# Kernel tuning notes

Hardware: AMD Instinct MI355X
Metric: run time of the kernel (lower is better)

Reference implementation:

```python
import jax, jax.numpy as jnp
import numpy as np

EDGE_THRESHOLD = 0.1
N_NODES, IN_DIM, OUT_DIM, EDGE_DIM = 512, 128, 128, 64
LN_EPS = 1e-5


def setup_inputs() -> dict:
    key = jax.random.key(0)
    ks = jax.random.split(key, 20)
    s = 0.05
    d_in2e = 2 * IN_DIM + EDGE_DIM
    return {
        "node_features": jax.random.normal(ks[0], (N_NODES, IN_DIM), jnp.float32),
        "W": jax.random.normal(ks[1], (N_NODES, N_NODES), jnp.float32),
        "M": jax.random.normal(ks[2], (N_NODES, N_NODES), jnp.float32),
        "edge_features": jax.random.normal(ks[3], (N_NODES, N_NODES, EDGE_DIM), jnp.float32),
        # node_mlp: Linear(in,out) -> ReLU -> Linear(out,out)
        "node_w1": jax.random.normal(ks[4], (IN_DIM, OUT_DIM), jnp.float32) * s,
        "node_b1": jnp.zeros((OUT_DIM,), jnp.float32),
        "node_w2": jax.random.normal(ks[5], (OUT_DIM, OUT_DIM), jnp.float32) * s,
        "node_b2": jnp.zeros((OUT_DIM,), jnp.float32),
        # directed_msg: Linear(2*in+edge_dim,out) -> ReLU -> Linear(out,out)
        "dir_w1": jax.random.normal(ks[6], (d_in2e, OUT_DIM), jnp.float32) * s,
        "dir_b1": jnp.zeros((OUT_DIM,), jnp.float32),
        "dir_w2": jax.random.normal(ks[7], (OUT_DIM, OUT_DIM), jnp.float32) * s,
        "dir_b2": jnp.zeros((OUT_DIM,), jnp.float32),
        # bidirected_msg: Linear(2*in,out) -> ReLU -> Linear(out,out)
        "bi_w1": jax.random.normal(ks[8], (2 * IN_DIM, OUT_DIM), jnp.float32) * s,
        "bi_b1": jnp.zeros((OUT_DIM,), jnp.float32),
        "bi_w2": jax.random.normal(ks[9], (OUT_DIM, OUT_DIM), jnp.float32) * s,
        "bi_b2": jnp.zeros((OUT_DIM,), jnp.float32),
        # LayerNorm(out)
        "ln_g": jnp.ones((OUT_DIM,), jnp.float32),
        "ln_b": jnp.zeros((OUT_DIM,), jnp.float32),
    }


def reference(node_features, W, M, edge_features,
              node_w1, node_b1, node_w2, node_b2,
              dir_w1, dir_b1, dir_w2, dir_b2,
              bi_w1, bi_b1, bi_w2, bi_b2,
              ln_g, ln_b):
    n, d = node_features.shape
    x = node_features

    # self path
    h_self = jax.nn.relu(x @ node_w1 + node_b1) @ node_w2 + node_b2

    # directed messages: msg[j,i] = MLP([x_j, x_i, e_{j,i}]), weight = |W[j,i]| masked.
    # First linear split by concat blocks to avoid materializing (n,n,2d+e).
    src = x @ dir_w1[:d]                 # (n,h)   parent/source term
    tgt = x @ dir_w1[d:2 * d]            # (n,h)   target term
    edg = jnp.einsum('jie,eh->jih', edge_features, dir_w1[2 * d:])  # (n,n,h)
    h1 = jax.nn.relu(src[:, None, :] + tgt[None, :, :] + edg + dir_b1)  # (n,n,h) [j,i]
    msg_d = h1 @ dir_w2 + dir_b2         # (n,n,out)
    absW = jnp.abs(W)
    wd = jnp.where(absW > EDGE_THRESHOLD, absW, 0.0)  # (n,n) [parent j, target i]
    h_dir = jnp.einsum('jio,ji->io', msg_d, wd)

    # bidirected messages: for node i, neighbors j: MLP([x_j, x_i]), weight = |M[i,j]| masked, j != i
    bsrc = x @ bi_w1[:d]
    btgt = x @ bi_w1[d:]
    h1b = jax.nn.relu(bsrc[:, None, :] + btgt[None, :, :] + bi_b1)  # (n,n,h) [j,i]
    msg_b = h1b @ bi_w2 + bi_b2
    absM = jnp.abs(M)
    wb = jnp.where(absM > EDGE_THRESHOLD, absM, 0.0)
    wb = wb * (1.0 - jnp.eye(n, dtype=wb.dtype))  # exclude self
    h_bi = jnp.einsum('jio,ij->io', msg_b, wb)

    h = h_self + h_dir + h_bi
    mu = jnp.mean(h, axis=-1, keepdims=True)
    var = jnp.mean(jnp.square(h - mu), axis=-1, keepdims=True)
    return (h - mu) * jax.lax.rsqrt(var + LN_EPS) * ln_g + ln_b
```

## Files before the change

### kernel.cpp

```cpp
#include <hip/hip_runtime.h>
#include <hip/hip_bf16.h>
#include <cstdint>

#define NN 512
#define DD 128
#define EE 64
#define THR 0.1f
#define NCHUNK 16

typedef __bf16 bf16x8 __attribute__((ext_vector_type(8)));
typedef float  f32x4  __attribute__((ext_vector_type(4)));

__global__ __launch_bounds__(256) void k_zero(float* __restrict__ p, int n)
{
    int i = blockIdx.x * 256 + threadIdx.x;
    if (i < n) p[i] = 0.f;
}

__global__ __launch_bounds__(128) void k_pre(
    const float* __restrict__ x,
    const float* __restrict__ dw1, const float* __restrict__ bw1,
    const float* __restrict__ nw1, const float* __restrict__ nb1,
    float* __restrict__ src, float* __restrict__ tgt,
    float* __restrict__ bsrc, float* __restrict__ btgt, float* __restrict__ hmid)
{
    const int i0 = blockIdx.x * 4;
    const int h  = threadIdx.x;
    const int which = blockIdx.y;
    const float* B; float* outp;
    switch (which) {
        case 0:  B = dw1;          outp = src;  break;
        case 1:  B = dw1 + DD*DD;  outp = tgt;  break;
        case 2:  B = bw1;          outp = bsrc; break;
        case 3:  B = bw1 + DD*DD;  outp = btgt; break;
        default: B = nw1;          outp = hmid; break;
    }
    __shared__ float sx[4][DD];
    for (int idx = h; idx < 4*DD; idx += DD)
        sx[idx >> 7][idx & 127] = x[i0*DD + idx];
    __syncthreads();
    float a0=0.f, a1=0.f, a2=0.f, a3=0.f;
    for (int k = 0; k < DD; ++k) {
        float w = B[k*DD + h];
        a0 = fmaf(sx[0][k], w, a0);
        a1 = fmaf(sx[1][k], w, a1);
        a2 = fmaf(sx[2][k], w, a2);
        a3 = fmaf(sx[3][k], w, a3);
    }
    if (which == 4) {
        float bb = nb1[h];
        a0 = fmaxf(a0+bb, 0.f); a1 = fmaxf(a1+bb, 0.f);
        a2 = fmaxf(a2+bb, 0.f); a3 = fmaxf(a3+bb, 0.f);
    }
    outp[(i0+0)*DD + h] = a0;
    outp[(i0+1)*DD + h] = a1;
    outp[(i0+2)*DD + h] = a2;
    outp[(i0+3)*DD + h] = a3;
}

__global__ __launch_bounds__(256, 2) void k_msg(
    const float* __restrict__ ef, const float* __restrict__ W,
    const float* __restrict__ M,
    const float* __restrict__ dw1, const float* __restrict__ db1,
    const float* __restrict__ src, const float* __restrict__ tgt,
    const float* __restrict__ bsrc, const float* __restrict__ btgt,
    const float* __restrict__ bb1,
    float* __restrict__ td_base, float* __restrict__ tb_base,
    float* __restrict__ wsum_d, float* __restrict__ wsum_b, int partial)
{
    __shared__ float smem[12800];
    const int bid  = blockIdx.x;
    const int role = bid & 1;
    const int sub  = bid >> 1;
    const int i0    = (sub & 31) * 16;
    const int jbase = (sub >> 5) * 32;
    const int chunk = sub >> 5;
    const int tid   = threadIdx.x;

    if (role == 0) {
        float* s_src = smem;
        float* s_wd  = smem + 4096;
        float* s_acc = smem + 4608;
        const int wave = tid >> 6, lane = tid & 63;
        const int lrow = lane & 15, lhi = lane >> 4;

        for (int idx = tid; idx < 32*DD; idx += 256)
            s_src[idx] = src[jbase*DD + idx];
        for (int idx = tid; idx < 32*16; idx += 256) {
            int jj = idx >> 4, il = idx & 15;
            float w = fabsf(W[(size_t)(jbase + jj)*NN + i0 + il]);
            s_wd[idx] = (w > THR) ? w : 0.0f;
        }

        bf16x8 bfrag[8][2];
        #pragma unroll
        for (int nf = 0; nf < 8; ++nf)
            #pragma unroll
            for (int kf = 0; kf < 2; ++kf) {
                bf16x8 t;
                #pragma unroll
                for (int e = 0; e < 8; ++e)
                    t[e] = (__bf16)dw1[(2*DD + kf*32 + lhi*8 + e)*DD + nf*16 + lrow];
                bfrag[nf][kf] = t;
            }

        float tpre[8][4];
        #pragma unroll
        for (int nf = 0; nf < 8; ++nf)
            #pragma unroll
            for (int r = 0; r < 4; ++r) {
                int hh = nf*16 + lrow;
                tpre[nf][r] = tgt[(i0 + lhi*4 + r)*DD + hh] + db1[hh];
            }

        float acc[8][4] = {};
        __syncthreads();

        const float* ebase = ef + ((size_t)(jbase + wave)*NN + i0)*EE + lrow*EE + lhi*8;
        const size_t jstep = (size_t)4 * NN * EE;
        float4 a0 = *(const float4*)(ebase + 0);
        float4 a1 = *(const float4*)(ebase + 4);
        float4 a2 = *(const float4*)(ebase + 32);
        float4 a3 = *(const float4*)(ebase + 36);

        #pragma unroll 2
        for (int it = 0; it < 8; ++it) {
            float4 c0 = a0, c1 = a1, c2 = a2, c3 = a3;
            if (it < 7) {
                const float* np = ebase + (size_t)(it + 1)*jstep;
                a0 = *(const float4*)(np + 0);
                a1 = *(const float4*)(np + 4);
                a2 = *(const float4*)(np + 32);
                a3 = *(const float4*)(np + 36);
            }
            const int jj = wave + it*4;

            bf16x8 af0, af1;
            af0[0]=(__bf16)c0.x; af0[1]=(__bf16)c0.y; af0[2]=(__bf16)c0.z; af0[3]=(__bf16)c0.w;
            af0[4]=(__bf16)c1.x; af0[5]=(__bf16)c1.y; af0[6]=(__bf16)c1.z; af0[7]=(__bf16)c1.w;
            af1[0]=(__bf16)c2.x; af1[1]=(__bf16)c2.y; af1[2]=(__bf16)c2.z; af1[3]=(__bf16)c2.w;
            af1[4]=(__bf16)c3.x; af1[5]=(__bf16)c3.y; af1[6]=(__bf16)c3.z; af1[7]=(__bf16)c3.w;

            float wdv[4];
            #pragma unroll
            for (int r = 0; r < 4; ++r) wdv[r] = s_wd[jj*16 + lhi*4 + r];

            #pragma unroll
            for (int nf = 0; nf < 8; ++nf) {
                f32x4 z = {0.f, 0.f, 0.f, 0.f};
                z = __builtin_amdgcn_mfma_f32_16x16x32_bf16(af0, bfrag[nf][0], z, 0, 0, 0);
                z = __builtin_amdgcn_mfma_f32_16x16x32_bf16(af1, bfrag[nf][1], z, 0, 0, 0);
                float sv = s_src[jj*DD + nf*16 + lrow];
                #pragma unroll
                for (int r = 0; r < 4; ++r) {
                    float v = z[r] + sv + tpre[nf][r];
                    acc[nf][r] = fmaf(wdv[r], fmaxf(v, 0.f), acc[nf][r]);
                }
            }
        }

        #pragma unroll
        for (int nf = 0; nf < 8; ++nf)
            #pragma unroll
            for (int r = 0; r < 4; ++r)
                s_acc[wave*16*DD + (lhi*4 + r)*DD + nf*16 + lrow] = acc[nf][r];
        __syncthreads();

        float* dst = td_base + (partial ? (size_t)chunk * (NN*DD) : 0);
        for (int idx = tid; idx < 16*DD; idx += 256) {
            int il = idx >> 7, hh = idx & 127;
            float s = s_acc[0*16*DD + il*DD + hh] + s_acc[1*16*DD + il*DD + hh]
                    + s_acc[2*16*DD + il*DD + hh] + s_acc[3*16*DD + il*DD + hh];
            int o = (i0 + il)*DD + hh;
            if (partial) dst[o] = s; else atomicAdd(&dst[o], s);
        }
        if (tid < 16) {
            float s = 0.f;
            #pragma unroll
            for (int jj = 0; jj < 32; ++jj) s += s_wd[jj*16 + tid];
            if (partial) wsum_d[chunk * NN + i0 + tid] = s;
            else         atomicAdd(&wsum_d[i0 + tid], s);
        }
    } else {
        float* s_wb = smem;
        float* s_bs = smem + 512;
        const int il = tid >> 4;
        const int hg = tid & 15;

        for (int idx = tid; idx < 16*32; idx += 256) {
            int r = idx >> 5, jj = idx & 31;
            float m = fabsf(M[(size_t)(i0 + r)*NN + jbase + jj]);
            float w = (m > THR) ? m : 0.f;
            if (i0 + r == jbase + jj) w = 0.f;
            s_wb[idx] = w;
        }
        for (int idx = tid; idx < 32*DD; idx += 256)
            s_bs[idx] = bsrc[jbase*DD + idx];
        __syncthreads();

        float bt[8], acc[8] = {};
        #pragma unroll
        for (int r = 0; r < 8; ++r) {
            int hh = hg*8 + r;
            bt[r] = btgt[(i0 + il)*DD + hh] + bb1[hh];
        }
        for (int jj = 0; jj < 32; ++jj) {
            float w = s_wb[il*32 + jj];
            const float* sp = &s_bs[jj*DD + hg*8];
            float4 v0 = *(const float4*)sp;
            float4 v1 = *(const float4*)(sp + 4);
            acc[0] = fmaf(w, fmaxf(v0.x + bt[0], 0.f), acc[0]);
            acc[1] = fmaf(w, fmaxf(v0.y + bt[1], 0.f), acc[1]);
            acc[2] = fmaf(w, fmaxf(v0.z + bt[2], 0.f), acc[2]);
            acc[3] = fmaf(w, fmaxf(v0.w + bt[3], 0.f), acc[3]);
            acc[4] = fmaf(w, fmaxf(v1.x + bt[4], 0.f), acc[4]);
            acc[5] = fmaf(w, fmaxf(v1.y + bt[5], 0.f), acc[5]);
            acc[6] = fmaf(w, fmaxf(v1.z + bt[6], 0.f), acc[6]);
            acc[7] = fmaf(w, fmaxf(v1.w + bt[7], 0.f), acc[7]);
        }
        float* dst = tb_base + (partial ? (size_t)chunk * (NN*DD) : 0);
        #pragma unroll
        for (int r = 0; r < 8; ++r) {
            int o = (i0 + il)*DD + hg*8 + r;
            if (partial) dst[o] = acc[r]; else atomicAdd(&dst[o], acc[r]);
        }
        if (tid < 16) {
            float s = 0.f;
            #pragma unroll
            for (int jj = 0; jj < 32; ++jj) s += s_wb[tid*32 + jj];
            if (partial) wsum_b[chunk * NN + i0 + tid] = s;
            else         atomicAdd(&wsum_b[i0 + tid], s);
        }
    }
}

__global__ __launch_bounds__(256) void k_final(
    const float* __restrict__ hmid, const float* __restrict__ nw2, const float* __restrict__ nb2,
    const float* __restrict__ td,   const float* __restrict__ dw2, const float* __restrict__ db2,
    const float* __restrict__ wsd,
    const float* __restrict__ tb,   const float* __restrict__ bw2, const float* __restrict__ bb2,
    const float* __restrict__ wsb,
    const float* __restrict__ lng,  const float* __restrict__ lnb,
    float* __restrict__ out, int cd, int cb, int wpart)
{
    const int tid = threadIdx.x;
    const int r   = tid >> 7;
    const int h   = tid & 127;
    const int row = blockIdx.x * 2 + r;
    const int o   = row * DD + h;

    __shared__ float sm[2][DD], sd[2][DD], sb[2][DD];
    __shared__ float red[4];

    float vm = hmid[o];
    float s1 = 0.f, s2 = 0.f;
    #pragma unroll 4
    for (int c = 0; c < cd; ++c) s1 += td[(size_t)c*(NN*DD) + o];
    #pragma unroll 4
    for (int c = 0; c < cb; ++c) s2 += tb[(size_t)c*(NN*DD) + o];
    sm[r][h] = vm; sd[r][h] = s1; sb[r][h] = s2;
    __syncthreads();

    float wsum_d_row, wsum_b_row;
    if (wpart) {
        float a = 0.f, b = 0.f;
        #pragma unroll
        for (int c = 0; c < NCHUNK; ++c) {
            a += wsd[c*NN + row];
            b += wsb[c*NN + row];
        }
        wsum_d_row = a; wsum_b_row = b;
    } else {
        wsum_d_row = wsd[row]; wsum_b_row = wsb[row];
    }

    float acc = nb2[h] + wsum_d_row*db2[h] + wsum_b_row*bb2[h];
    #pragma unroll 4
    for (int k = 0; k < DD; ++k) {
        acc += sm[r][k]*nw2[k*DD + h] + sd[r][k]*dw2[k*DD + h] + sb[r][k]*bw2[k*DD + h];
    }

    const int wid = tid >> 6;
    float s = acc;
    #pragma unroll
    for (int off = 32; off > 0; off >>= 1) s += __shfl_down(s, off);
    if ((tid & 63) == 0) red[wid] = s;
    __syncthreads();
    float mu = (red[2*r] + red[2*r + 1]) * (1.0f/128.0f);
    float dv = acc - mu;
    float q  = dv * dv;
    __syncthreads();
    #pragma unroll
    for (int off = 32; off > 0; off >>= 1) q += __shfl_down(q, off);
    if ((tid & 63) == 0) red[wid] = q;
    __syncthreads();
    float var = (red[2*r] + red[2*r + 1]) * (1.0f/128.0f);
    out[o] = dv * rsqrtf(var + 1e-5f) * lng[h] + lnb[h];
}

extern "C" void kernel_launch(void* const* d_in, const int* in_sizes, int n_in,
                              void* d_out, int out_size, void* d_ws, size_t ws_size,
                              hipStream_t stream)
{
    (void)in_sizes; (void)n_in; (void)out_size;
    const float* x   = (const float*)d_in[0];
    const float* W   = (const float*)d_in[1];
    const float* M   = (const float*)d_in[2];
    const float* ef  = (const float*)d_in[3];
    const float* nw1 = (const float*)d_in[4];
    const float* nb1 = (const float*)d_in[5];
    const float* nw2 = (const float*)d_in[6];
    const float* nb2 = (const float*)d_in[7];
    const float* dw1 = (const float*)d_in[8];
    const float* db1 = (const float*)d_in[9];
    const float* dw2 = (const float*)d_in[10];
    const float* db2 = (const float*)d_in[11];
    const float* bw1 = (const float*)d_in[12];
    const float* bb1 = (const float*)d_in[13];
    const float* bw2 = (const float*)d_in[14];
    const float* bb2 = (const float*)d_in[15];
    const float* lng = (const float*)d_in[16];
    const float* lnb = (const float*)d_in[17];
    float* out = (float*)d_out;
    float* ws  = (float*)d_ws;

    const size_t TD = (size_t)NN * DD;
    const size_t WS_PART = (size_t)NCHUNK * NN;
    const size_t PART_FLOATS = 32*TD + 2*WS_PART + 5*TD;
    const int partial = (ws_size >= PART_FLOATS * 4) ? 1 : 0;

    float *t_dir, *t_bi, *wsd, *wsb, *base;
    if (partial) {
        t_dir = ws;
        t_bi  = ws + 16*TD;
        wsd   = ws + 32*TD;
        wsb   = wsd + WS_PART;
        base  = wsb + WS_PART;
    } else {
        t_dir = ws;
        t_bi  = ws + TD;
        wsd   = ws + 2*TD;
        wsb   = wsd + 512;
        base  = ws + 2*TD + 1024;
        int nz = (int)(2*TD + 1024);
        k_zero<<<(nz + 255)/256, 256, 0, stream>>>(ws, nz);
    }
    float* src  = base;
    float* tgt  = base + TD;
    float* bsrc = base + 2*TD;
    float* btgt = base + 3*TD;
    float* hmid = base + 4*TD;

    k_pre  <<<dim3(NN/4, 5), 128, 0, stream>>>(x, dw1, bw1, nw1, nb1,
                                               src, tgt, bsrc, btgt, hmid);
    k_msg  <<<1024, 256, 0, stream>>>(ef, W, M, dw1, db1, src, tgt,
                                      bsrc, btgt, bb1,
                                      t_dir, t_bi, wsd, wsb, partial);
    const int cd = partial ? NCHUNK : 1;
    k_final<<<NN/2, 256, 0, stream>>>(hmid, nw2, nb2, t_dir, dw2, db2, wsd,
                                      t_bi, bw2, bb2, wsb, lng, lnb, out,
                                      cd, cd, partial);
}
```

Measured before the change: 61.39 us.

## Stage edge-feature tiles into LDS asynchronously and split hidden columns across waves

```diff
diff --git a/kernel.cpp b/kernel.cpp
--- a/kernel.cpp
+++ b/kernel.cpp
@@ -10,6 +10,12 @@
 
 typedef __bf16 bf16x8 __attribute__((ext_vector_type(8)));
 typedef float  f32x4  __attribute__((ext_vector_type(4)));
+
+__device__ __forceinline__ void stage16(const float* g, float* l) {
+    __builtin_amdgcn_global_load_lds(
+        (const __attribute__((address_space(1))) uint32_t*)g,
+        (__attribute__((address_space(3))) uint32_t*)l, 16, 0, 0);
+}
 
 __global__ __launch_bounds__(256) void k_zero(float* __restrict__ p, int n)
 {
@@ -58,7 +64,7 @@
     outp[(i0+3)*DD + h] = a3;
 }
 
-__global__ __launch_bounds__(256, 2) void k_msg(
+__global__ __launch_bounds__(256, 4) void k_msg(
     const float* __restrict__ ef, const float* __restrict__ W,
     const float* __restrict__ M,
     const float* __restrict__ dw1, const float* __restrict__ db1,
@@ -68,7 +74,7 @@
     float* __restrict__ td_base, float* __restrict__ tb_base,
     float* __restrict__ wsum_d, float* __restrict__ wsum_b, int partial)
 {
-    __shared__ float smem[12800];
+    __shared__ float smem[8704];
     const int bid  = blockIdx.x;
     const int role = bid & 1;
     const int sub  = bid >> 1;
@@ -78,102 +84,131 @@
     const int tid   = threadIdx.x;
 
     if (role == 0) {
-        float* s_src = smem;
-        float* s_wd  = smem + 4096;
-        float* s_acc = smem + 4608;
-        const int wave = tid >> 6, lane = tid & 63;
-        const int lrow = lane & 15, lhi = lane >> 4;
-
-        for (int idx = tid; idx < 32*DD; idx += 256)
-            s_src[idx] = src[jbase*DD + idx];
+        float* stg   = smem;
+        float* s_src = smem + 4096;
+        float* s_wd  = smem + 8192;
+        const int wv   = tid >> 6;
+        const int l    = tid & 63;
+        const int lrow = l & 15, lhi = l >> 4;
+
+        const int srow = tid >> 4;
+        const int sst  = tid & 15;
+        const int slog = (sst & 8) | ((sst & 7) ^ (srow & 7));
+        const float* gsrc0 = ef + ((size_t)jbase*NN + i0 + srow)*EE + slog*4;
+        float* ldst = stg + tid*4;
+
+        #pragma unroll
+        for (int t = 0; t < 4; ++t)
+            stage16(gsrc0 + (size_t)t*NN*EE, ldst + t*1024);
+
+        for (int idx = tid; idx < 32*DD/4; idx += 256)
+            ((float4*)s_src)[idx] = ((const float4*)(src + jbase*DD))[idx];
         for (int idx = tid; idx < 32*16; idx += 256) {
-            int jj = idx >> 4, il = idx & 15;
-            float w = fabsf(W[(size_t)(jbase + jj)*NN + i0 + il]);
+            int jj = idx >> 4, ii = idx & 15;
+            float w = fabsf(W[(size_t)(jbase + jj)*NN + i0 + ii]);
             s_wd[idx] = (w > THR) ? w : 0.0f;
         }
 
-        bf16x8 bfrag[8][2];
-        #pragma unroll
-        for (int nf = 0; nf < 8; ++nf)
+        bf16x8 bfrag[2][2];
+        #pragma unroll
+        for (int nfl = 0; nfl < 2; ++nfl)
             #pragma unroll
             for (int kf = 0; kf < 2; ++kf) {
                 bf16x8 t;
                 #pragma unroll
                 for (int e = 0; e < 8; ++e)
-                    t[e] = (__bf16)dw1[(2*DD + kf*32 + lhi*8 + e)*DD + nf*16 + lrow];
-                bfrag[nf][kf] = t;
+                    t[e] = (__bf16)dw1[(2*DD + kf*32 + lhi*8 + e)*DD + (wv*2+nfl)*16 + lrow];
+                bfrag[nfl][kf] = t;
             }
-
-        float tpre[8][4];
-        #pragma unroll
-        for (int nf = 0; nf < 8; ++nf)
+        float tpre[2][4];
+        #pragma unroll
+        for (int nfl = 0; nfl < 2; ++nfl)
             #pragma unroll
             for (int r = 0; r < 4; ++r) {
-                int hh = nf*16 + lrow;
-                tpre[nf][r] = tgt[(i0 + lhi*4 + r)*DD + hh] + db1[hh];
+                int hh = (wv*2+nfl)*16 + lrow;
+                tpre[nfl][r] = tgt[(i0 + lhi*4 + r)*DD + hh] + db1[hh];
             }
 
-        float acc[8][4] = {};
+        int ro[4];
+        #pragma unroll
+        for (int h2 = 0; h2 < 2; ++h2)
+            #pragma unroll
+            for (int q = 0; q < 2; ++q) {
+                int slot = h2*8 + lhi*2 + q;
+                int st = (slot & 8) | ((slot & 7) ^ (lrow & 7));
+                ro[h2*2 + q] = lrow*64 + st*4;
+            }
+
+        float acc[2][4] = {};
         __syncthreads();
 
-        const float* ebase = ef + ((size_t)(jbase + wave)*NN + i0)*EE + lrow*EE + lhi*8;
-        const size_t jstep = (size_t)4 * NN * EE;
-        float4 a0 = *(const float4*)(ebase + 0);
-        float4 a1 = *(const float4*)(ebase + 4);
-        float4 a2 = *(const float4*)(ebase + 32);
-        float4 a3 = *(const float4*)(ebase + 36);
-
-        #pragma unroll 2
-        for (int it = 0; it < 8; ++it) {
-            float4 c0 = a0, c1 = a1, c2 = a2, c3 = a3;
-            if (it < 7) {
-                const float* np = ebase + (size_t)(it + 1)*jstep;
-                a0 = *(const float4*)(np + 0);
-                a1 = *(const float4*)(np + 4);
-                a2 = *(const float4*)(np + 32);
-                a3 = *(const float4*)(np + 36);
+#define READ_TILE(BUF)                                                        \
+        {                                                                     \
+            const float* buf_ = (BUF);                                        \
+            float4 f0 = *(const float4*)(buf_ + ro[0]);                       \
+            float4 f1 = *(const float4*)(buf_ + ro[1]);                       \
+            float4 f2 = *(const float4*)(buf_ + ro[2]);                       \
+            float4 f3 = *(const float4*)(buf_ + ro[3]);                       \
+            af0[0]=(__bf16)f0.x; af0[1]=(__bf16)f0.y;                         \
+            af0[2]=(__bf16)f0.z; af0[3]=(__bf16)f0.w;                         \
+            af0[4]=(__bf16)f1.x; af0[5]=(__bf16)f1.y;                         \
+            af0[6]=(__bf16)f1.z; af0[7]=(__bf16)f1.w;                         \
+            af1[0]=(__bf16)f2.x; af1[1]=(__bf16)f2.y;                         \
+            af1[2]=(__bf16)f2.z; af1[3]=(__bf16)f2.w;                         \
+            af1[4]=(__bf16)f3.x; af1[5]=(__bf16)f3.y;                         \
+            af1[6]=(__bf16)f3.z; af1[7]=(__bf16)f3.w;                         \
+        }
+
+#define MATH_TILE(T)                                                          \
+        {                                                                     \
+            float wdv[4];                                                     \
+            _Pragma("unroll")                                                 \
+            for (int r = 0; r < 4; ++r) wdv[r] = s_wd[(T)*16 + lhi*4 + r];    \
+            _Pragma("unroll")                                                 \
+            for (int nfl = 0; nfl < 2; ++nfl) {                               \
+                f32x4 z = {0.f, 0.f, 0.f, 0.f};                               \
+                z = __builtin_amdgcn_mfma_f32_16x16x32_bf16(af0, bfrag[nfl][0], z, 0, 0, 0); \
+                z = __builtin_amdgcn_mfma_f32_16x16x32_bf16(af1, bfrag[nfl][1], z, 0, 0, 0); \
+                float sv = s_src[(T)*DD + (wv*2+nfl)*16 + lrow];              \
+                _Pragma("unroll")                                             \
+                for (int r = 0; r < 4; ++r) {                                 \
+                    float v = z[r] + sv + tpre[nfl][r];                       \
+                    acc[nfl][r] = fmaf(wdv[r], fmaxf(v, 0.f), acc[nfl][r]);   \
+                }                                                             \
+            }                                                                 \
+        }
+
+        bf16x8 af0, af1;
+        for (int t = 0; t < 28; ++t) {
+            asm volatile("s_waitcnt vmcnt(3)" ::: "memory");
+            __builtin_amdgcn_sched_barrier(0);
+            __builtin_amdgcn_s_barrier();
+            __builtin_amdgcn_sched_barrier(0);
+            READ_TILE(stg + (t & 3)*1024);
+            __builtin_amdgcn_sched_barrier(0);
+            __builtin_amdgcn_s_barrier();
+            stage16(gsrc0 + (size_t)(t + 4)*NN*EE, ldst + (t & 3)*1024);
+            MATH_TILE(t);
+        }
+        asm volatile("s_waitcnt vmcnt(0)" ::: "memory");
+        __builtin_amdgcn_sched_barrier(0);
+        __builtin_amdgcn_s_barrier();
+        for (int t = 28; t < 32; ++t) {
+            READ_TILE(stg + (t & 3)*1024);
+            MATH_TILE(t);
+        }
+#undef READ_TILE
+#undef MATH_TILE
+
+        float* dst = td_base + (partial ? (size_t)chunk * (NN*DD) : 0);
+        #pragma unroll
+        for (int nfl = 0; nfl < 2; ++nfl)
+            #pragma unroll
+            for (int r = 0; r < 4; ++r) {
+                int o = (i0 + lhi*4 + r)*DD + (wv*2+nfl)*16 + lrow;
+                if (partial) dst[o] = acc[nfl][r];
+                else         atomicAdd(&dst[o], acc[nfl][r]);
             }
-            const int jj = wave + it*4;
-
-            bf16x8 af0, af1;
-            af0[0]=(__bf16)c0.x; af0[1]=(__bf16)c0.y; af0[2]=(__bf16)c0.z; af0[3]=(__bf16)c0.w;
-            af0[4]=(__bf16)c1.x; af0[5]=(__bf16)c1.y; af0[6]=(__bf16)c1.z; af0[7]=(__bf16)c1.w;
-            af1[0]=(__bf16)c2.x; af1[1]=(__bf16)c2.y; af1[2]=(__bf16)c2.z; af1[3]=(__bf16)c2.w;
-            af1[4]=(__bf16)c3.x; af1[5]=(__bf16)c3.y; af1[6]=(__bf16)c3.z; af1[7]=(__bf16)c3.w;
-
-            float wdv[4];
-            #pragma unroll
-            for (int r = 0; r < 4; ++r) wdv[r] = s_wd[jj*16 + lhi*4 + r];
-
-            #pragma unroll
-            for (int nf = 0; nf < 8; ++nf) {
-                f32x4 z = {0.f, 0.f, 0.f, 0.f};
-                z = __builtin_amdgcn_mfma_f32_16x16x32_bf16(af0, bfrag[nf][0], z, 0, 0, 0);
-                z = __builtin_amdgcn_mfma_f32_16x16x32_bf16(af1, bfrag[nf][1], z, 0, 0, 0);
-                float sv = s_src[jj*DD + nf*16 + lrow];
-                #pragma unroll
-                for (int r = 0; r < 4; ++r) {
-                    float v = z[r] + sv + tpre[nf][r];
-                    acc[nf][r] = fmaf(wdv[r], fmaxf(v, 0.f), acc[nf][r]);
-                }
-            }
-        }
-
-        #pragma unroll
-        for (int nf = 0; nf < 8; ++nf)
-            #pragma unroll
-            for (int r = 0; r < 4; ++r)
-                s_acc[wave*16*DD + (lhi*4 + r)*DD + nf*16 + lrow] = acc[nf][r];
-        __syncthreads();
-
-        float* dst = td_base + (partial ? (size_t)chunk * (NN*DD) : 0);
-        for (int idx = tid; idx < 16*DD; idx += 256) {
-            int il = idx >> 7, hh = idx & 127;
-            float s = s_acc[0*16*DD + il*DD + hh] + s_acc[1*16*DD + il*DD + hh]
-                    + s_acc[2*16*DD + il*DD + hh] + s_acc[3*16*DD + il*DD + hh];
-            int o = (i0 + il)*DD + hh;
-            if (partial) dst[o] = s; else atomicAdd(&dst[o], s);
-        }
         if (tid < 16) {
             float s = 0.f;
             #pragma unroll
```

Result: faster. 54.87 us, median of 2 (-10.6%).
